# Kernel tuning notes

Measured on AMD Instinct MI355X. Metric: run time of the kernel, lower is better.

Reference implementation:

```python
import jax, jax.numpy as jnp
import numpy as np

_B = 128          # quantization block size
FP8_MAX = 448.0   # finfo(float8_e4m3fn).max


def _quantize_weight_block(w):
    """w: [N, K] fp32 -> (fp8 weight [N,K], per-block scale [N/128, K/128])."""
    N, K = w.shape
    blk = w.reshape(N // _B, _B, K // _B, _B).transpose(0, 2, 1, 3)  # [n,k,128,128]
    amax = jnp.abs(blk).max(axis=(-2, -1))
    scale = jnp.maximum(amax / FP8_MAX, 1e-12).astype(jnp.float32)   # [n,k]
    q = jnp.clip(blk / scale[:, :, None, None], -FP8_MAX, FP8_MAX).astype(jnp.float8_e4m3fn)
    wq = q.transpose(0, 2, 1, 3).reshape(N, K)
    return wq, scale


def _dequant_weight(wq, scale):
    N, K = wq.shape
    blk = wq.reshape(N // _B, _B, K // _B, _B).astype(jnp.float32)
    blk = blk * scale[:, None, :, None]
    return blk.reshape(N, K)


def _fake_quant_act(x):
    """Per-token, per-128-column-group fp8 fake quantization. x: [M, K]."""
    M, K = x.shape
    xg = x.reshape(M, K // _B, _B)
    amax = jnp.abs(xg).max(axis=-1, keepdims=True)
    scale = jnp.maximum(amax / FP8_MAX, 1e-12)
    xq = jnp.clip(xg / scale, -FP8_MAX, FP8_MAX).astype(jnp.float8_e4m3fn).astype(jnp.float32)
    return (xq * scale).reshape(M, K)


def _fq_linear(x, wq, wscale):
    # fake-quant activation, dequant weight, high-precision GEMM
    return _fake_quant_act(x) @ _dequant_weight(wq, wscale).T


def setup_inputs() -> dict:
    key = jax.random.key(0)
    k0, k1, k2, k3 = jax.random.split(key, 4)
    M, H, I = 4096, 4096, 14336
    x = jax.random.normal(k0, (M, H), dtype=jnp.float32)
    gate_w = jax.random.normal(k1, (I, H), dtype=jnp.float32) * 0.05
    up_w = jax.random.normal(k2, (I, H), dtype=jnp.float32) * 0.05
    down_w = jax.random.normal(k3, (H, I), dtype=jnp.float32) * 0.05
    gq, gs = _quantize_weight_block(gate_w)
    uq, us = _quantize_weight_block(up_w)
    dq, ds = _quantize_weight_block(down_w)
    return {
        "x": x,
        "gate_weight": gq, "gate_weight_scale": gs,
        "up_weight": uq, "up_weight_scale": us,
        "down_weight": dq, "down_weight_scale": ds,
    }


def reference(x, gate_weight, gate_weight_scale, up_weight, up_weight_scale,
              down_weight, down_weight_scale):
    gate_out = _fq_linear(x, gate_weight, gate_weight_scale)
    up_out = _fq_linear(x, up_weight, up_weight_scale)
    hidden = jax.nn.silu(gate_out) * up_out
    return _fq_linear(hidden, down_weight, down_weight_scale)
```

## Files before the change

### kernel.cpp

```cpp
#include <hip/hip_runtime.h>

typedef float floatx4 __attribute__((ext_vector_type(4)));
typedef long longx2 __attribute__((ext_vector_type(2)));
typedef unsigned int u32;
typedef unsigned char u8;

#define MDIM 4096
#define HDIM 4096
#define IDIM 14336
#define FP8MAX 448.0f

__device__ __forceinline__ int swz4(int r) { return (r ^ (r >> 2)) & 3; }
__device__ __forceinline__ int frag_off(int row, int quad) {
  return (row << 6) + ((quad ^ swz4(row)) << 4);
}

__device__ __forceinline__ void gload16(const u8* g, u8* l) {
  __builtin_amdgcn_global_load_lds((const __attribute__((address_space(1))) u32*)g,
                                   (__attribute__((address_space(3))) u32*)l, 16, 0, 0);
}

__global__ void detect_dtype(const unsigned int* __restrict__ w, int* __restrict__ flag) {
  if (threadIdx.x == 0 && blockIdx.x == 0) {
    bool f32 = true, b16 = true;
    for (int i = 0; i < 64; ++i) {
      const unsigned int v = w[i];
      if (v & 0xFFFFFu) f32 = false;
      if ((v & 0xFu) || ((v >> 16) & 0xFu)) b16 = false;
    }
    *flag = f32 ? 2 : (b16 ? 1 : 0);
  }
}

__device__ __forceinline__ float bfu(unsigned int bits16) {
  union { unsigned int u; float f; } c;
  c.u = bits16 << 16;
  return c.f;
}

__device__ __forceinline__ unsigned int pack2(unsigned int lo, unsigned int hi) {
  int pk = __builtin_amdgcn_cvt_pk_fp8_f32(bfu(lo & 0xFFFFu), bfu(lo >> 16), 0, false);
  pk = __builtin_amdgcn_cvt_pk_fp8_f32(bfu(hi & 0xFFFFu), bfu(hi >> 16), pk, true);
  return (unsigned int)pk;
}

__global__ __launch_bounds__(256) void conv_w(const void* __restrict__ src,
                                              unsigned char* __restrict__ dst,
                                              const int* __restrict__ flag_p) {
  const int flag = *flag_p;
  if (flag == 0) return;
  const long t = (long)blockIdx.x * 256 + threadIdx.x;
  uint4 out;
  if (flag == 2) {
    const float4* s = (const float4*)src;
    unsigned int o[4];
#pragma unroll
    for (int p = 0; p < 4; ++p) {
      const float4 v = s[t * 4 + p];
      int pk = __builtin_amdgcn_cvt_pk_fp8_f32(v.x, v.y, 0, false);
      pk = __builtin_amdgcn_cvt_pk_fp8_f32(v.z, v.w, pk, true);
      o[p] = (unsigned int)pk;
    }
    out = make_uint4(o[0], o[1], o[2], o[3]);
  } else {
    const uint4* s = (const uint4*)src;
    const uint4 a = s[t * 2], b = s[t * 2 + 1];
    out = make_uint4(pack2(a.x, a.y), pack2(a.z, a.w),
                     pack2(b.x, b.y), pack2(b.z, b.w));
  }
  ((uint4*)dst)[t] = out;
}

__global__ __launch_bounds__(256) void fq_act(const float* __restrict__ x,
                                              unsigned char* __restrict__ xq,
                                              float* __restrict__ xsT) {
  const int tid = threadIdx.x;
  const int lane = tid & 63, w = tid >> 6;
  const int g = blockIdx.x * 4 + w;
  const int row = g >> 5, kb = g & 31;

  const float2 v = ((const float2*)(x + (size_t)row * HDIM + kb * 128))[lane];
  float amax = fmaxf(fabsf(v.x), fabsf(v.y));
#pragma unroll
  for (int off = 1; off < 64; off <<= 1)
    amax = fmaxf(amax, __shfl_xor(amax, off, 64));

  const float scale = fmaxf(amax / FP8MAX, 1e-12f);
  const float q0 = fminf(fmaxf(v.x / scale, -FP8MAX), FP8MAX);
  const float q1 = fminf(fmaxf(v.y / scale, -FP8MAX), FP8MAX);
  const int pk = __builtin_amdgcn_cvt_pk_fp8_f32(q0, q1, 0, false);
  ((unsigned short*)(xq + (size_t)row * HDIM + kb * 128))[lane] = (unsigned short)(pk & 0xFFFF);
  if (lane == 0) xsT[(size_t)kb * MDIM + row] = scale;
}

__global__ __launch_bounds__(256, 2)
void dual_gemm_silu_fq(const u8* __restrict__ xq, const float* __restrict__ xsT,
                       const u8* __restrict__ gw_cv, const u8* __restrict__ gw_raw,
                       const float* __restrict__ gs,
                       const u8* __restrict__ uw_cv, const u8* __restrict__ uw_raw,
                       const float* __restrict__ us,
                       u8* __restrict__ hq, float* __restrict__ hsT,
                       const int* __restrict__ flag_p, const int use_conv) {
  __shared__ __align__(16) u8 lds[49152];

  const int tid = threadIdx.x;
  const int lane = tid & 63, wid = tid >> 6;
  const int quad = lane >> 4, l16 = lane & 15;

  const int bid0 = blockIdx.x;
  const int bid = (bid0 & 7) * 448 + (bid0 >> 3);
  const int mi = bid & 31, ni = bid >> 5;
  const size_t m0 = (size_t)mi << 7, n0 = (size_t)ni << 7;

  const u8* gw = gw_raw;
  const u8* uw = uw_raw;
  if (use_conv) {
    if (*flag_p != 0) { gw = gw_cv; uw = uw_cv; }
  }

  const u8* baseA = xq + m0 * HDIM;
  const u8* baseG = gw + n0 * HDIM;
  const u8* baseU = uw + n0 * HDIM;

  const int r16 = lane >> 2, slot = lane & 3;
  u32 srcoff[2], dstoff[2];
#pragma unroll
  for (int i = 0; i < 2; ++i) {
    const int row = wid * 32 + i * 16 + r16;
    srcoff[i] = (u32)(row * HDIM) + (u32)((slot ^ swz4(row)) << 4);
    dstoff[i] = (u32)(wid * 2048 + i * 1024);
  }

  int offA[2], offB[8];
#pragma unroll
  for (int mt = 0; mt < 2; ++mt) offA[mt] = frag_off(wid * 32 + mt * 16 + l16, quad);
#pragma unroll
  for (int nt = 0; nt < 8; ++nt) offB[nt] = frag_off(nt * 16 + l16, quad);

  floatx4 accG[2][8], accU[2][8];
#pragma unroll
  for (int mt = 0; mt < 2; ++mt)
#pragma unroll
    for (int nt = 0; nt < 8; ++nt) {
      accG[mt][nt] = {0.f, 0.f, 0.f, 0.f};
      accU[mt][nt] = {0.f, 0.f, 0.f, 0.f};
    }

  auto STAGE = [&](int t, int b) {
    const u32 ko = (u32)t << 6;
    const u32 bo = (u32)b << 13;
#pragma unroll
    for (int i = 0; i < 2; ++i) {
      gload16(baseA + srcoff[i] + ko, &lds[bo + dstoff[i]]);
      gload16(baseG + srcoff[i] + ko, &lds[16384u + bo + dstoff[i]]);
      gload16(baseU + srcoff[i] + ko, &lds[32768u + bo + dstoff[i]]);
    }
  };

  auto HALF = [&](int b) {
    const u8* bufA = lds + (b << 13);
    const u8* bufG = lds + 16384 + (b << 13);
    const u8* bufU = lds + 32768 + (b << 13);
    longx2 aF[2];
#pragma unroll
    for (int mt = 0; mt < 2; ++mt) aF[mt] = *(const longx2*)(bufA + offA[mt]);

    __builtin_amdgcn_s_setprio(1);
#pragma unroll
    for (int nt = 0; nt < 8; ++nt) {
      const longx2 bF = *(const longx2*)(bufG + offB[nt]);
#pragma unroll
      for (int mt = 0; mt < 2; ++mt) {
        accG[mt][nt] = __builtin_amdgcn_mfma_f32_16x16x32_fp8_fp8(aF[mt][0], bF[0], accG[mt][nt], 0, 0, 0);
        accG[mt][nt] = __builtin_amdgcn_mfma_f32_16x16x32_fp8_fp8(aF[mt][1], bF[1], accG[mt][nt], 0, 0, 0);
      }
    }
#pragma unroll
    for (int nt = 0; nt < 8; ++nt) {
      const longx2 bF = *(const longx2*)(bufU + offB[nt]);
#pragma unroll
      for (int mt = 0; mt < 2; ++mt) {
        accU[mt][nt] = __builtin_amdgcn_mfma_f32_16x16x32_fp8_fp8(aF[mt][0], bF[0], accU[mt][nt], 0, 0, 0);
        accU[mt][nt] = __builtin_amdgcn_mfma_f32_16x16x32_fp8_fp8(aF[mt][1], bF[1], accU[mt][nt], 0, 0, 0);
      }
    }
    __builtin_amdgcn_s_setprio(0);
  };

  STAGE(0, 0);
  asm volatile("s_waitcnt vmcnt(0)" ::: "memory");
  __builtin_amdgcn_s_barrier();

  float prG[2][4], prU[2][4];

  for (int kb = 0; kb < 32; ++kb) {
    const float sg = gs[ni * 32 + kb];
    const float su = us[ni * 32 + kb];
    float cG[2][4], cU[2][4];
#pragma unroll
    for (int mt = 0; mt < 2; ++mt) {
      const float4 v = *(const float4*)(xsT + (size_t)kb * MDIM + m0 + wid * 32 + mt * 16 + quad * 4);
      cG[mt][0] = v.x * sg; cG[mt][1] = v.y * sg; cG[mt][2] = v.z * sg; cG[mt][3] = v.w * sg;
      cU[mt][0] = v.x * su; cU[mt][1] = v.y * su; cU[mt][2] = v.z * su; cU[mt][3] = v.w * su;
    }
    if (kb) {
      float rG[2][4], rU[2][4];
#pragma unroll
      for (int mt = 0; mt < 2; ++mt)
#pragma unroll
        for (int r = 0; r < 4; ++r) {
          rG[mt][r] = prG[mt][r] / cG[mt][r];
          rU[mt][r] = prU[mt][r] / cU[mt][r];
        }
#pragma unroll
      for (int mt = 0; mt < 2; ++mt)
#pragma unroll
        for (int nt = 0; nt < 8; ++nt)
#pragma unroll
          for (int r = 0; r < 4; ++r) {
            accG[mt][nt][r] *= rG[mt][r];
            accU[mt][nt][r] *= rU[mt][r];
          }
    }
#pragma unroll
    for (int mt = 0; mt < 2; ++mt)
#pragma unroll
      for (int r = 0; r < 4; ++r) { prG[mt][r] = cG[mt][r]; prU[mt][r] = cU[mt][r]; }

    STAGE(2 * kb + 1, 1);
    HALF(0);
    asm volatile("s_waitcnt vmcnt(0)" ::: "memory");
    __builtin_amdgcn_s_barrier();
    if (kb + 1 < 32) STAGE(2 * kb + 2, 0);
    HALF(1);
    asm volatile("s_waitcnt vmcnt(0)" ::: "memory");
    __builtin_amdgcn_s_barrier();
  }

#pragma unroll
  for (int mt = 0; mt < 2; ++mt)
#pragma unroll
    for (int nt = 0; nt < 8; ++nt)
#pragma unroll
      for (int r = 0; r < 4; ++r) {
        accG[mt][nt][r] *= prG[mt][r];
        accU[mt][nt][r] *= prU[mt][r];
      }

  u8* ot = lds;
#pragma unroll
  for (int mt = 0; mt < 2; ++mt) {
    float h[8][4];
    float amax[4] = {0.f, 0.f, 0.f, 0.f};
#pragma unroll
    for (int nt = 0; nt < 8; ++nt)
#pragma unroll
      for (int r = 0; r < 4; ++r) {
        const float gv = accG[mt][nt][r];
        const float uv = accU[mt][nt][r];
        const float hv = (gv / (1.f + __expf(-gv))) * uv;
        h[nt][r] = hv;
        amax[r] = fmaxf(amax[r], fabsf(hv));
      }
#pragma unroll
    for (int off = 1; off < 16; off <<= 1)
#pragma unroll
      for (int r = 0; r < 4; ++r)
        amax[r] = fmaxf(amax[r], __shfl_xor(amax[r], off, 64));

    float scale[4];
#pragma unroll
    for (int r = 0; r < 4; ++r) scale[r] = fmaxf(amax[r] / FP8MAX, 1e-12f);

    const int rowl = wid * 32 + mt * 16 + quad * 4;
    if (l16 == 0) {
#pragma unroll
      for (int r = 0; r < 4; ++r)
        hsT[(size_t)ni * MDIM + m0 + rowl + r] = scale[r];
    }
#pragma unroll
    for (int nt = 0; nt < 8; ++nt)
#pragma unroll
      for (int r = 0; r < 4; ++r) {
        const float q = fminf(fmaxf(h[nt][r] / scale[r], -FP8MAX), FP8MAX);
        const int pk = __builtin_amdgcn_cvt_pk_fp8_f32(q, 0.f, 0, false);
        ot[(rowl + r) * 128 + nt * 16 + l16] = (u8)(pk & 0xFF);
      }
  }
  __syncthreads();
  {
    const int row = tid >> 1, half = tid & 1;
    const uint4* s = (const uint4*)(ot + row * 128 + half * 64);
    uint4* d = (uint4*)(hq + (m0 + row) * IDIM + n0 + half * 64);
#pragma unroll
    for (int i = 0; i < 4; ++i) d[i] = s[i];
  }
}

__global__ __launch_bounds__(256, 2)
void gemm_down(const u8* __restrict__ hq, const float* __restrict__ hsT,
               const u8* __restrict__ dw_cv, const u8* __restrict__ dw_raw,
               const float* __restrict__ dsc, float* __restrict__ out,
               const int* __restrict__ flag_p, const int use_conv) {
  __shared__ __align__(16) u8 lds[32768];

  const int tid = threadIdx.x;
  const int lane = tid & 63, wid = tid >> 6;
  const int quad = lane >> 4, l16 = lane & 15;

  const int bid0 = blockIdx.x;
  const int bid = (bid0 & 7) * 128 + (bid0 >> 3);
  const int mi = bid & 31, ni = bid >> 5;
  const size_t m0 = (size_t)mi << 7, n0 = (size_t)ni << 7;

  const u8* dw = dw_raw;
  if (use_conv) {
    if (*flag_p != 0) dw = dw_cv;
  }

  const u8* baseA = hq + m0 * IDIM;
  const u8* baseB = dw + n0 * IDIM;

  const int r16 = lane >> 2, slot = lane & 3;
  u32 srcoff[2], dstoff[2];
#pragma unroll
  for (int i = 0; i < 2; ++i) {
    const int row = wid * 32 + i * 16 + r16;
    srcoff[i] = (u32)(row * IDIM) + (u32)((slot ^ swz4(row)) << 4);
    dstoff[i] = (u32)(wid * 2048 + i * 1024);
  }

  int offA[2], offB[8];
#pragma unroll
  for (int mt = 0; mt < 2; ++mt) offA[mt] = frag_off(wid * 32 + mt * 16 + l16, quad);
#pragma unroll
  for (int nt = 0; nt < 8; ++nt) offB[nt] = frag_off(nt * 16 + l16, quad);

  floatx4 acc[2][8];
#pragma unroll
  for (int mt = 0; mt < 2; ++mt)
#pragma unroll
    for (int nt = 0; nt < 8; ++nt) acc[mt][nt] = {0.f, 0.f, 0.f, 0.f};

  auto STAGE = [&](int t, int b) {
    const u32 ko = (u32)t << 6;
    const u32 bo = (u32)b << 13;
#pragma unroll
    for (int i = 0; i < 2; ++i) {
      gload16(baseA + srcoff[i] + ko, &lds[bo + dstoff[i]]);
      gload16(baseB + srcoff[i] + ko, &lds[16384u + bo + dstoff[i]]);
    }
  };

  auto HALF = [&](int b) {
    const u8* bufA = lds + (b << 13);
    const u8* bufB = lds + 16384 + (b << 13);
    longx2 aF[2];
#pragma unroll
    for (int mt = 0; mt < 2; ++mt) aF[mt] = *(const longx2*)(bufA + offA[mt]);
    __builtin_amdgcn_s_setprio(1);
#pragma unroll
    for (int nt = 0; nt < 8; ++nt) {
      const longx2 bF = *(const longx2*)(bufB + offB[nt]);
#pragma unroll
      for (int mt = 0; mt < 2; ++mt) {
        acc[mt][nt] = __builtin_amdgcn_mfma_f32_16x16x32_fp8_fp8(aF[mt][0], bF[0], acc[mt][nt], 0, 0, 0);
        acc[mt][nt] = __builtin_amdgcn_mfma_f32_16x16x32_fp8_fp8(aF[mt][1], bF[1], acc[mt][nt], 0, 0, 0);
      }
    }
    __builtin_amdgcn_s_setprio(0);
  };

  STAGE(0, 0);
  asm volatile("s_waitcnt vmcnt(0)" ::: "memory");
  __builtin_amdgcn_s_barrier();

  float prS[2][4];
  for (int kb = 0; kb < 112; ++kb) {
    const float sd = dsc[ni * 112 + kb];
    float cS[2][4];
#pragma unroll
    for (int mt = 0; mt < 2; ++mt) {
      const float4 v = *(const float4*)(hsT + (size_t)kb * MDIM + m0 + wid * 32 + mt * 16 + quad * 4);
      cS[mt][0] = v.x * sd; cS[mt][1] = v.y * sd; cS[mt][2] = v.z * sd; cS[mt][3] = v.w * sd;
    }
    if (kb) {
      float rS[2][4];
#pragma unroll
      for (int mt = 0; mt < 2; ++mt)
#pragma unroll
        for (int r = 0; r < 4; ++r) rS[mt][r] = prS[mt][r] / cS[mt][r];
#pragma unroll
      for (int mt = 0; mt < 2; ++mt)
#pragma unroll
        for (int nt = 0; nt < 8; ++nt)
#pragma unroll
          for (int r = 0; r < 4; ++r) acc[mt][nt][r] *= rS[mt][r];
    }
#pragma unroll
    for (int mt = 0; mt < 2; ++mt)
#pragma unroll
      for (int r = 0; r < 4; ++r) prS[mt][r] = cS[mt][r];

    STAGE(2 * kb + 1, 1);
    HALF(0);
    asm volatile("s_waitcnt vmcnt(0)" ::: "memory");
    __builtin_amdgcn_s_barrier();
    if (kb + 1 < 112) STAGE(2 * kb + 2, 0);
    HALF(1);
    asm volatile("s_waitcnt vmcnt(0)" ::: "memory");
    __builtin_amdgcn_s_barrier();
  }

#pragma unroll
  for (int mt = 0; mt < 2; ++mt) {
    const int rowl = wid * 32 + mt * 16 + quad * 4;
#pragma unroll
    for (int nt = 0; nt < 8; ++nt)
#pragma unroll
      for (int r = 0; r < 4; ++r)
        out[(m0 + rowl + r) * (size_t)HDIM + n0 + nt * 16 + l16] = acc[mt][nt][r] * prS[mt][r];
  }
}

extern "C" void kernel_launch(void* const* d_in, const int* in_sizes, int n_in,
                              void* d_out, int out_size, void* d_ws, size_t ws_size,
                              hipStream_t stream) {
  const float* x   = (const float*)d_in[0];
  const void* gw_s = d_in[1];
  const float* gs  = (const float*)d_in[2];
  const void* uw_s = d_in[3];
  const float* us  = (const float*)d_in[4];
  const void* dw_s = d_in[5];
  const float* dsc = (const float*)d_in[6];
  float* out       = (float*)d_out;

  const size_t NW = (size_t)IDIM * HDIM;

  unsigned char* ws = (unsigned char*)d_ws;
  unsigned char* xq = ws;
  float* xsT = (float*)(ws + 16777216);
  unsigned char* hq  = ws + 17301504;
  float* hsT = (float*)(ws + 76021760);
  unsigned char* gwq = ws + 77856768;
  unsigned char* uwq = ws + 136577024;
  unsigned char* dwq = gwq;
  int* flag = (int*)(ws + 195297280);

  const bool fits = ws_size >= (size_t)195297284;
  const int use_conv = fits ? 1 : 0;

  const int convBlocks = (int)(NW / (16 * 256));

  if (fits) {
    detect_dtype<<<1, 64, 0, stream>>>((const unsigned int*)gw_s, flag);
    conv_w<<<convBlocks, 256, 0, stream>>>(gw_s, gwq, flag);
    conv_w<<<convBlocks, 256, 0, stream>>>(uw_s, uwq, flag);
  }
  fq_act<<<(MDIM * (HDIM / 128)) / 4, 256, 0, stream>>>(x, xq, xsT);
  dual_gemm_silu_fq<<<(MDIM / 128) * (IDIM / 128), 256, 0, stream>>>(
      xq, xsT, gwq, (const unsigned char*)gw_s, gs,
      uwq, (const unsigned char*)uw_s, us, hq, hsT, flag, use_conv);
  if (fits) {
    conv_w<<<convBlocks, 256, 0, stream>>>(dw_s, dwq, flag);
  }
  gemm_down<<<(MDIM / 128) * (HDIM / 128), 256, 0, stream>>>(
      hq, hsT, dwq, (const unsigned char*)dw_s, dsc, out, flag, use_conv);
}
```

Before: 1.983 ms.

## Triple-buffer LDS K-tiles with two-deep prefetch and prefetch block scales

Both GEMM kernels move from a double buffer that drained all loads (vmcnt(0)) every half-step to a three-slot LDS ring. Loads run two stages ahead, and partial vmcnt waits let the next tiles stay in flight during MFMA work. The per-k-block activation and weight scales are loaded one iteration early. The rescale ratio is also factored so fewer divisions are needed per block. This raises LDS use per block (72KB for the dual GEMM), which tightens occupancy headroom, and it adds an extra barrier per half-step.

After: 1.886 ms. 1.05x faster.

```diff
diff --git a/kernel.cpp b/kernel.cpp
--- a/kernel.cpp
+++ b/kernel.cpp
@@ -101,7 +101,7 @@
                        const float* __restrict__ us,
                        u8* __restrict__ hq, float* __restrict__ hsT,
                        const int* __restrict__ flag_p, const int use_conv) {
-  __shared__ __align__(16) u8 lds[49152];
+  __shared__ __align__(16) u8 lds[73728];
 
   const int tid = threadIdx.x;
   const int lane = tid & 63, wid = tid >> 6;
@@ -148,19 +148,20 @@
 
   auto STAGE = [&](int t, int b) {
     const u32 ko = (u32)t << 6;
-    const u32 bo = (u32)b << 13;
+    u8* lb = lds + b * 24576;
 #pragma unroll
     for (int i = 0; i < 2; ++i) {
-      gload16(baseA + srcoff[i] + ko, &lds[bo + dstoff[i]]);
-      gload16(baseG + srcoff[i] + ko, &lds[16384u + bo + dstoff[i]]);
-      gload16(baseU + srcoff[i] + ko, &lds[32768u + bo + dstoff[i]]);
+      gload16(baseA + srcoff[i] + ko, lb + dstoff[i]);
+      gload16(baseG + srcoff[i] + ko, lb + 8192u + dstoff[i]);
+      gload16(baseU + srcoff[i] + ko, lb + 16384u + dstoff[i]);
     }
   };
 
   auto HALF = [&](int b) {
-    const u8* bufA = lds + (b << 13);
-    const u8* bufG = lds + 16384 + (b << 13);
-    const u8* bufU = lds + 32768 + (b << 13);
+    const u8* lb = lds + b * 24576;
+    const u8* bufA = lb;
+    const u8* bufG = lb + 8192;
+    const u8* bufU = lb + 16384;
     longx2 aF[2];
 #pragma unroll
     for (int mt = 0; mt < 2; ++mt) aF[mt] = *(const longx2*)(bufA + offA[mt]);
@@ -187,65 +188,93 @@
     __builtin_amdgcn_s_setprio(0);
   };
 
+  const float* xrow = xsT + m0 + wid * 32 + quad * 4;
+  float4 xv0 = *(const float4*)(xrow);
+  float4 xv1 = *(const float4*)(xrow + 16);
+  float sgn = gs[ni * 32];
+  float sun = us[ni * 32];
+
   STAGE(0, 0);
-  asm volatile("s_waitcnt vmcnt(0)" ::: "memory");
-  __builtin_amdgcn_s_barrier();
-
-  float prG[2][4], prU[2][4];
+  STAGE(1, 1);
+
+  float prX[2][4];
+  float sgp = 1.f, sup = 1.f;
+  int cb = 0;
 
   for (int kb = 0; kb < 32; ++kb) {
-    const float sg = gs[ni * 32 + kb];
-    const float su = us[ni * 32 + kb];
-    float cG[2][4], cU[2][4];
-#pragma unroll
-    for (int mt = 0; mt < 2; ++mt) {
-      const float4 v = *(const float4*)(xsT + (size_t)kb * MDIM + m0 + wid * 32 + mt * 16 + quad * 4);
-      cG[mt][0] = v.x * sg; cG[mt][1] = v.y * sg; cG[mt][2] = v.z * sg; cG[mt][3] = v.w * sg;
-      cU[mt][0] = v.x * su; cU[mt][1] = v.y * su; cU[mt][2] = v.z * su; cU[mt][3] = v.w * su;
-    }
+    float cx[2][4];
+    cx[0][0] = xv0.x; cx[0][1] = xv0.y; cx[0][2] = xv0.z; cx[0][3] = xv0.w;
+    cx[1][0] = xv1.x; cx[1][1] = xv1.y; cx[1][2] = xv1.z; cx[1][3] = xv1.w;
+    const float sgc = sgn, suc = sun;
     if (kb) {
-      float rG[2][4], rU[2][4];
+      const float rgs = sgp / sgc, rus = sup / suc;
 #pragma unroll
       for (int mt = 0; mt < 2; ++mt)
 #pragma unroll
         for (int r = 0; r < 4; ++r) {
-          rG[mt][r] = prG[mt][r] / cG[mt][r];
-          rU[mt][r] = prU[mt][r] / cU[mt][r];
+          const float cm = prX[mt][r] / cx[mt][r];
+          const float rg = cm * rgs, ru = cm * rus;
+#pragma unroll
+          for (int nt = 0; nt < 8; ++nt) {
+            accG[mt][nt][r] *= rg;
+            accU[mt][nt][r] *= ru;
+          }
         }
-#pragma unroll
-      for (int mt = 0; mt < 2; ++mt)
-#pragma unroll
-        for (int nt = 0; nt < 8; ++nt)
-#pragma unroll
-          for (int r = 0; r < 4; ++r) {
-            accG[mt][nt][r] *= rG[mt][r];
-            accU[mt][nt][r] *= rU[mt][r];
-          }
     }
 #pragma unroll
     for (int mt = 0; mt < 2; ++mt)
 #pragma unroll
-      for (int r = 0; r < 4; ++r) { prG[mt][r] = cG[mt][r]; prU[mt][r] = cU[mt][r]; }
-
-    STAGE(2 * kb + 1, 1);
-    HALF(0);
-    asm volatile("s_waitcnt vmcnt(0)" ::: "memory");
-    __builtin_amdgcn_s_barrier();
-    if (kb + 1 < 32) STAGE(2 * kb + 2, 0);
-    HALF(1);
-    asm volatile("s_waitcnt vmcnt(0)" ::: "memory");
-    __builtin_amdgcn_s_barrier();
+      for (int r = 0; r < 4; ++r) prX[mt][r] = cx[mt][r];
+    sgp = sgc; sup = suc;
+
+    if (kb + 1 < 32) {
+      const float* xn = xsT + (size_t)(kb + 1) * MDIM + m0 + wid * 32 + quad * 4;
+      xv0 = *(const float4*)(xn);
+      xv1 = *(const float4*)(xn + 16);
+      sgn = gs[ni * 32 + kb + 1];
+      sun = us[ni * 32 + kb + 1];
+    }
+
+    {
+      int sb = cb + 2; if (sb >= 3) sb -= 3;
+      if (kb < 31) {
+        STAGE(2 * kb + 2, sb);
+        asm volatile("s_waitcnt vmcnt(12)" ::: "memory");
+      } else {
+        asm volatile("s_waitcnt vmcnt(6)" ::: "memory");
+      }
+      __builtin_amdgcn_s_barrier();
+      HALF(cb);
+      __builtin_amdgcn_s_barrier();
+      cb = cb + 1; if (cb >= 3) cb -= 3;
+    }
+    {
+      int sb = cb + 2; if (sb >= 3) sb -= 3;
+      if (kb < 31) {
+        STAGE(2 * kb + 3, sb);
+        asm volatile("s_waitcnt vmcnt(12)" ::: "memory");
+      } else {
+        asm volatile("s_waitcnt vmcnt(0)" ::: "memory");
+      }
+      __builtin_amdgcn_s_barrier();
+      HALF(cb);
+      __builtin_amdgcn_s_barrier();
+      cb = cb + 1; if (cb >= 3) cb -= 3;
+    }
   }
 
 #pragma unroll
   for (int mt = 0; mt < 2; ++mt)
 #pragma unroll
-    for (int nt = 0; nt < 8; ++nt)
-#pragma unroll
-      for (int r = 0; r < 4; ++r) {
-        accG[mt][nt][r] *= prG[mt][r];
-        accU[mt][nt][r] *= prU[mt][r];
-      }
+    for (int r = 0; r < 4; ++r) {
+      const float fg = prX[mt][r] * sgp;
+      const float fu = prX[mt][r] * sup;
+#pragma unroll
+      for (int nt = 0; nt < 8; ++nt) {
+        accG[mt][nt][r] *= fg;
+        accU[mt][nt][r] *= fu;
+      }
+    }
 
   u8* ot = lds;
 #pragma unroll
@@ -302,7 +331,7 @@
                const u8* __restrict__ dw_cv, const u8* __restrict__ dw_raw,
                const float* __restrict__ dsc, float* __restrict__ out,
                const int* __restrict__ flag_p, const int use_conv) {
-  __shared__ __align__(16) u8 lds[32768];
+  __shared__ __align__(16) u8 lds[49152];
 
   const int tid = threadIdx.x;
   const int lane = tid & 63, wid = tid >> 6;
@@ -344,24 +373,23 @@
 
   auto STAGE = [&](int t, int b) {
     const u32 ko = (u32)t << 6;
-    const u32 bo = (u32)b << 13;
+    u8* lb = lds + b * 16384;
 #pragma unroll
     for (int i = 0; i < 2; ++i) {
-      gload16(baseA + srcoff[i] + ko, &lds[bo + dstoff[i]]);
-      gload16(baseB + srcoff[i] + ko, &lds[16384u + bo + dstoff[i]]);
+      gload16(baseA + srcoff[i] + ko, lb + dstoff[i]);
+      gload16(baseB + srcoff[i] + ko, lb + 8192u + dstoff[i]);
     }
   };
 
   auto HALF = [&](int b) {
-    const u8* bufA = lds + (b << 13);
-    const u8* bufB = lds + 16384 + (b << 13);
+    const u8* lb = lds + b * 16384;
     longx2 aF[2];
 #pragma unroll
-    for (int mt = 0; mt < 2; ++mt) aF[mt] = *(const longx2*)(bufA + offA[mt]);
+    for (int mt = 0; mt < 2; ++mt) aF[mt] = *(const longx2*)(lb + offA[mt]);
     __builtin_amdgcn_s_setprio(1);
 #pragma unroll
     for (int nt = 0; nt < 8; ++nt) {
-      const longx2 bF = *(const longx2*)(bufB + offB[nt]);
+      const longx2 bF = *(const longx2*)(lb + 8192 + offB[nt]);
 #pragma unroll
       for (int mt = 0; mt < 2; ++mt) {
         acc[mt][nt] = __builtin_amdgcn_mfma_f32_16x16x32_fp8_fp8(aF[mt][0], bF[0], acc[mt][nt], 0, 0, 0);
@@ -371,45 +399,73 @@
     __builtin_amdgcn_s_setprio(0);
   };
 
+  const float* hrow = hsT + m0 + wid * 32 + quad * 4;
+  float4 xv0 = *(const float4*)(hrow);
+  float4 xv1 = *(const float4*)(hrow + 16);
+  float sdn = dsc[ni * 112];
+
   STAGE(0, 0);
-  asm volatile("s_waitcnt vmcnt(0)" ::: "memory");
-  __builtin_amdgcn_s_barrier();
-
-  float prS[2][4];
+  STAGE(1, 1);
+
+  float prX[2][4];
+  float sdp = 1.f;
+  int cb = 0;
+
   for (int kb = 0; kb < 112; ++kb) {
-    const float sd = dsc[ni * 112 + kb];
-    float cS[2][4];
-#pragma unroll
-    for (int mt = 0; mt < 2; ++mt) {
-      const float4 v = *(const float4*)(hsT + (size_t)kb * MDIM + m0 + wid * 32 + mt * 16 + quad * 4);
-      cS[mt][0] = v.x * sd; cS[mt][1] = v.y * sd; cS[mt][2] = v.z * sd; cS[mt][3] = v.w * sd;
-    }
+    float cx[2][4];
+    cx[0][0] = xv0.x; cx[0][1] = xv0.y; cx[0][2] = xv0.z; cx[0][3] = xv0.w;
+    cx[1][0] = xv1.x; cx[1][1] = xv1.y; cx[1][2] = xv1.z; cx[1][3] = xv1.w;
+    const float sdc = sdn;
     if (kb) {
-      float rS[2][4];
+      const float rds = sdp / sdc;
 #pragma unroll
       for (int mt = 0; mt < 2; ++mt)
 #pragma unroll
-        for (int r = 0; r < 4; ++r) rS[mt][r] = prS[mt][r] / cS[mt][r];
-#pragma unroll
-      for (int mt = 0; mt < 2; ++mt)
-#pragma unroll
-        for (int nt = 0; nt < 8; ++nt)
-#pragma unroll
-          for (int r = 0; r < 4; ++r) acc[mt][nt][r] *= rS[mt][r];
+        for (int r = 0; r < 4; ++r) {
+          const float rr = (prX[mt][r] / cx[mt][r]) * rds;
+#pragma unroll
+          for (int nt = 0; nt < 8; ++nt) acc[mt][nt][r] *= rr;
+        }
     }
 #pragma unroll
     for (int mt = 0; mt < 2; ++mt)
 #pragma unroll
-      for (int r = 0; r < 4; ++r) prS[mt][r] = cS[mt][r];
-
-    STAGE(2 * kb + 1, 1);
-    HALF(0);
-    asm volatile("s_waitcnt vmcnt(0)" ::: "memory");
-    __builtin_amdgcn_s_barrier();
-    if (kb + 1 < 112) STAGE(2 * kb + 2, 0);
-    HALF(1);
-    asm volatile("s_waitcnt vmcnt(0)" ::: "memory");
-    __builtin_amdgcn_s_barrier();
+      for (int r = 0; r < 4; ++r) prX[mt][r] = cx[mt][r];
+    sdp = sdc;
+
+    if (kb + 1 < 112) {
+      const float* xn = hsT + (size_t)(kb + 1) * MDIM + m0 + wid * 32 + quad * 4;
+      xv0 = *(const float4*)(xn);
+      xv1 = *(const float4*)(xn + 16);
+      sdn = dsc[ni * 112 + kb + 1];
+    }
+
+    {
+      int sb = cb + 2; if (sb >= 3) sb -= 3;
+      if (kb < 111) {
+        STAGE(2 * kb + 2, sb);
+        asm volatile("s_waitcnt vmcnt(8)" ::: "memory");
+      } else {
+        asm volatile("s_waitcnt vmcnt(4)" ::: "memory");
+      }
+      __builtin_amdgcn_s_barrier();
+      HALF(cb);
+      __builtin_amdgcn_s_barrier();
+      cb = cb + 1; if (cb >= 3) cb -= 3;
+    }
+    {
+      int sb = cb + 2; if (sb >= 3) sb -= 3;
+      if (kb < 111) {
+        STAGE(2 * kb + 3, sb);
+        asm volatile("s_waitcnt vmcnt(8)" ::: "memory");
+      } else {
+        asm volatile("s_waitcnt vmcnt(0)" ::: "memory");
+      }
+      __builtin_amdgcn_s_barrier();
+      HALF(cb);
+      __builtin_amdgcn_s_barrier();
+      cb = cb + 1; if (cb >= 3) cb -= 3;
+    }
   }
 
 #pragma unroll
@@ -419,7 +475,8 @@
     for (int nt = 0; nt < 8; ++nt)
 #pragma unroll
       for (int r = 0; r < 4; ++r)
-        out[(m0 + rowl + r) * (size_t)HDIM + n0 + nt * 16 + l16] = acc[mt][nt][r] * prS[mt][r];
+        out[(m0 + rowl + r) * (size_t)HDIM + n0 + nt * 16 + l16] =
+            acc[mt][nt][r] * prX[mt][r] * sdp;
   }
 }
 
```
